# Kernel optimization log

Measured on AMD Instinct MI355X. Metric: run time of the kernel, lower is better.

Reference implementation:

```python
import jax, jax.numpy as jnp
import numpy as np

B, L = 64, 200
NQ = 1024          # n_question == output_dim
NPID = 4096
D = 256            # q_embed_dim
H = 512            # hidden_dim
Q = 1024           # output_dim
L2 = 1e-05


def setup_inputs() -> dict:
    key = jax.random.key(0)
    ks = jax.random.split(key, 20)
    q_data = jax.random.randint(ks[0], (B, L), 1, NQ + 1)          # question ids in [1, NQ]
    ans = jax.random.randint(ks[1], (B, L), 0, 2)
    qa_data = q_data + NQ * ans                                     # encoded (q, answer)
    pid_data = jax.random.randint(ks[2], (B, L), 0, NPID + 1)
    matrix = jax.random.uniform(ks[3], (Q, Q), jnp.float32) * 0.05  # p_c_relations
    u = jax.random.uniform(ks[4], (B, L))
    target = jnp.where(u < 0.1, -1.0, jnp.where(u < 0.55, 0.0, 1.0)).astype(jnp.float32)
    s = 0.05
    q_emb = jax.random.normal(ks[5], (NQ + 1, D), jnp.float32) * s
    qa_emb = jax.random.normal(ks[6], (2, D), jnp.float32) * s
    q_emb_diff = jax.random.normal(ks[7], (NQ + 1, D), jnp.float32) * s
    qa_emb_diff = jax.random.normal(ks[8], (2 * NQ + 1, D), jnp.float32) * s
    diff_parm = jax.random.normal(ks[9], (NPID + 1, 1), jnp.float32) * s
    gs = 1.0 / np.sqrt(H).astype(np.float32)
    w_ih = jax.random.uniform(ks[10], (3 * H, 2 * D), jnp.float32, -gs, gs)
    w_hh = jax.random.uniform(ks[11], (3 * H, H), jnp.float32, -gs, gs)
    b_ih = jax.random.uniform(ks[12], (3 * H,), jnp.float32, -gs, gs)
    b_hh = jax.random.uniform(ks[13], (3 * H,), jnp.float32, -gs, gs)
    fc_w = jax.random.normal(ks[14], (Q, H), jnp.float32) * 0.02
    fc_b = jnp.zeros((Q,), jnp.float32)
    return dict(q_data=q_data, qa_data=qa_data, pid_data=pid_data, matrix=matrix,
                target=target, q_emb=q_emb, qa_emb=qa_emb, q_emb_diff=q_emb_diff,
                qa_emb_diff=qa_emb_diff, diff_parm=diff_parm, w_ih=w_ih, w_hh=w_hh,
                b_ih=b_ih, b_hh=b_hh, fc_w=fc_w, fc_b=fc_b)


def _gru(x, w_ih, w_hh, b_ih, b_hh):
    # PyTorch GRU, single layer, batch_first. x: [B, L, In]
    xg = jnp.einsum('bli,gi->blg', x, w_ih) + b_ih          # [B, L, 3H]
    def step(h, xg_t):
        hg = h @ w_hh.T + b_hh
        xr, xz, xn = jnp.split(xg_t, 3, axis=-1)
        hr, hz, hn = jnp.split(hg, 3, axis=-1)
        r = jax.nn.sigmoid(xr + hr)
        z = jax.nn.sigmoid(xz + hz)
        n = jnp.tanh(xn + r * hn)
        h_new = (1.0 - z) * n + z * h
        return h_new, h_new
    h0 = jnp.zeros((x.shape[0], w_hh.shape[1]), x.dtype)
    _, hs = jax.lax.scan(step, h0, xg.transpose(1, 0, 2))
    return hs.transpose(1, 0, 2)                             # [B, L, H]


def reference(q_data, qa_data, pid_data, matrix, target, q_emb, qa_emb,
              q_emb_diff, qa_emb_diff, diff_parm, w_ih, w_hh, b_ih, b_hh,
              fc_w, fc_b):
    q_embed = q_emb[q_data]                                  # [B, L, D]
    qa = (qa_data - q_data) // NQ                            # answer in {0,1}
    qa_embed = qa_emb[qa] + q_embed
    pid_embed = diff_parm[pid_data]                          # [B, L, 1]
    q_embed2 = q_embed + pid_embed * q_emb_diff[q_data]
    qa_embed2 = qa_embed + pid_embed * qa_emb_diff[qa]
    c_reg = (pid_embed ** 2).sum() * L2

    x = jnp.concatenate([qa_embed2, q_embed2], axis=-1)      # [B, L, 2D]
    gru_out = _gru(x, w_ih, w_hh, b_ih, b_hh)
    gru_out = jnp.einsum('blh,qh->blq', gru_out, fc_w) + fc_b  # [B, L, Q]

    got = jnp.einsum('blq,kq->blk', gru_out, matrix)         # [B, L, Q]
    master = jnp.where(got >= 0.4, 1.0, got)                 # threshold-to-1 only
    # mastery of the question asked at step t: master[b, t, q-1]
    mvals = jnp.take_along_axis(master, (q_data - 1)[..., None], axis=2)[..., 0]  # [B, L]

    f32 = jnp.float32
    eq = (q_data[:, :, None] == q_data[:, None, :]).astype(f32)   # [B, t, k]
    t_idx = jnp.arange(L)
    tri_strict = (t_idx[:, None] > t_idx[None, :]).astype(f32)    # k < t
    tri_incl = (t_idx[:, None] >= t_idx[None, :]).astype(f32)     # k <= t
    mast = (mvals == 1.0).astype(f32)
    notm = (mvals == 0.0).astype(f32)
    qa1 = (qa == 1).astype(f32)
    qa0 = 1.0 - qa1
    base = eq * tri_strict                                        # [B, L, L]
    mc = jnp.einsum('btk,bk->bt', base, qa1 * mast)   # master_correct
    mi = jnp.einsum('btk,bk->bt', base, qa0 * mast)   # master_incorrect
    nmc = jnp.einsum('btk,bk->bt', base, qa0 * notm)  # no_master_correct
    aa = jnp.einsum('btk,tk->bt', eq, tri_incl)       # answered_all (>= 1)

    arB = jnp.arange(B)
    idx = q_data - 1

    def dina_step(carry, xs):
        guess, slip = carry                            # [B, Q] each
        i_t, m_t, qa_t, mc_t, mi_t, nmc_t, aa_t = xs   # [B] each
        g_upd = jnp.where(m_t == 1.0, mc_t / aa_t,
                          jnp.where(qa_t == 0, 1.0 - nmc_t / aa_t, nmc_t / aa_t))
        upd_slip = (m_t == 1.0) & (qa_t == 0)
        new_g = jnp.where(upd_slip, guess[arB, i_t], g_upd)
        new_s = jnp.where(upd_slip, mi_t / aa_t, slip[arB, i_t])
        guess = guess.at[arB, i_t].set(new_g)
        slip = slip.at[arB, i_t].set(new_s)
        p = (1.0 - new_s) * (m_t * new_g + (1.0 - new_s) * (1.0 - m_t))
        return (guess, slip), p

    init = (jnp.zeros((B, Q), f32), jnp.zeros((B, Q), f32))
    xs = (idx.T, mvals.T, qa.T, mc.T, mi.T, nmc.T, aa.T)
    _, ps = jax.lax.scan(dina_step, init, xs)          # [L, B]
    preds = ps.T.reshape(-1)                           # [B*L]

    labels = target.reshape(-1)
    mask = labels > -0.9
    preds_d = jax.lax.stop_gradient(preds)             # torch detaches via torch.tensor()
    mse_sum = (((preds_d - labels) ** 2) * mask.astype(f32)).sum()
    loss = mse_sum + c_reg
    return (loss, jax.nn.sigmoid(preds_d), mask.sum())
```

## Files before the change

kernel.cpp:

```cpp
#include <hip/hip_runtime.h>
#include <hip/hip_bf16.h>
#include <math.h>

#define BB 64
#define LL 200
#define NQ 1024
#define DD 256
#define HH 512
#define QQ 1024
#define G3 1536
#define BL 12800
#define GBLK 256

#define OFF_ACC   ((size_t)0)
#define OFF_CELLS ((size_t)16)
#define OFF_HA    ((size_t)1056)
#define OFF_AQ    (OFF_HA + 65536)
#define OFF_DQ    (OFF_AQ + 1574400)
#define OFF_BQA   (OFF_DQ + 1574400)
#define OFF_CQA   (OFF_BQA + 3072)
#define OFF_WSUM  (OFF_CQA + 3072)
#define OFF_FCWT  (OFF_WSUM + 393216)
#define OFF_M2    (OFF_FCWT + 524288)
#define OFF_MB    (OFF_M2 + 524288)
#define OFF_XG    (OFF_MB + 1024)
#define OFF_GRUT  (OFF_XG + 19660800)
#define OFF_QINT  (OFF_GRUT + 6553600)
#define OFF_QAINT (OFF_QINT + 12800)
#define OFF_PIDF  (OFF_QAINT + 12800)
#define OFF_MVAL  (OFF_PIDF + 12800)
#define OFF_MC    (OFF_MVAL + 12800)
#define OFF_MI    (OFF_MC + 12800)
#define OFF_NMC   (OFF_MI + 12800)
#define OFF_AA    (OFF_NMC + 12800)
#define OFF_PREDS (OFF_AA + 12800)

typedef float f32x4 __attribute__((ext_vector_type(4)));

__device__ __forceinline__ float wave_sum64(float v) {
    #pragma unroll
    for (int o = 32; o > 0; o >>= 1) v += __shfl_down(v, o, 64);
    return v;
}

__device__ __forceinline__ f32x4 llc_load4(const float* p) {
    f32x4 v;
    asm volatile("global_load_dwordx4 %0, %1, off sc0 sc1" : "=v"(v) : "v"(p));
    return v;
}
__device__ __forceinline__ void llc_wait2(f32x4& a, f32x4& b) {
    asm volatile("s_waitcnt vmcnt(0)" : "+v"(a), "+v"(b));
}
__device__ __forceinline__ void llc_store1(float* p, float v) {
    asm volatile("global_store_dword %0, %1, off sc0 sc1" :: "v"(p), "v"(v) : "memory");
}

__device__ __forceinline__ float quad_sum(float v) {
    float t1 = __int_as_float(__builtin_amdgcn_update_dpp(
        0, __float_as_int(v), 0xB1, 0xF, 0xF, true));
    v += t1;
    float t2 = __int_as_float(__builtin_amdgcn_update_dpp(
        0, __float_as_int(v), 0x4E, 0xF, 0xF, true));
    return v + t2;
}

__global__ __launch_bounds__(256) void prep_meta(
    const int* __restrict__ q_data, const int* __restrict__ qa_data,
    const int* __restrict__ pid_data, const float* __restrict__ diff_parm,
    int* __restrict__ qint, int* __restrict__ qaint, float* __restrict__ pidf,
    float* __restrict__ acc)
{
    int r = blockIdx.x * 256 + threadIdx.x;
    float pp = 0.f;
    if (r < BL) {
        int q = q_data[r];
        qint[r] = q;
        qaint[r] = (qa_data[r] - q) / NQ;
        float pid = diff_parm[pid_data[r]];
        pidf[r] = pid;
        pp = pid * pid;
    }
    pp = wave_sum64(pp);
    __shared__ float sm[4];
    int lane = threadIdx.x & 63, w = threadIdx.x >> 6;
    if (lane == 0) sm[w] = pp;
    __syncthreads();
    if (threadIdx.x == 0) atomicAdd(&acc[0], sm[0] + sm[1] + sm[2] + sm[3]);
}

__global__ __launch_bounds__(256) void wsum_kernel(const float* __restrict__ w_ih,
                                                   float* __restrict__ wsum)
{
    int g = blockIdx.x, d = threadIdx.x;
    wsum[(size_t)g * DD + d] = w_ih[(size_t)g * 2 * DD + d] + w_ih[(size_t)g * 2 * DD + DD + d];
}

__global__ __launch_bounds__(256) void gemm_nt_dual(
    const float* __restrict__ A0, const float* __restrict__ A1, int lda,
    const float* __restrict__ B0, const float* __restrict__ B1, int ldb0, int ldb1,
    float* __restrict__ C0, float* __restrict__ C1, int ldc,
    int M, int N, int K,
    const float* __restrict__ bias0, const float* __restrict__ bias1)
{
    const int z = blockIdx.z;
    const float* A = z ? A1 : A0;
    const float* B = z ? B1 : B0;
    float* C = z ? C1 : C0;
    const int ldb = z ? ldb1 : ldb0;
    const float* bias = z ? bias1 : bias0;

    __shared__ float As[16][129];
    __shared__ float Bs[16][65];
    const int bm = blockIdx.y * 128, bn = blockIdx.x * 64;
    const int tid = threadIdx.x;
    const int tx = tid & 15, ty = tid >> 4;
    const int mm = tid >> 4, kk = tid & 15;
    float acc[8][4] = {};
    float ar[8], br[4];
    #pragma unroll
    for (int i = 0; i < 8; ++i) {
        int m = bm + mm + 16 * i;
        ar[i] = (m < M) ? A[(size_t)m * lda + kk] : 0.f;
    }
    #pragma unroll
    for (int i = 0; i < 4; ++i) {
        int n = bn + mm + 16 * i;
        br[i] = (n < N) ? B[(size_t)n * ldb + kk] : 0.f;
    }
    for (int k0 = 0; k0 < K; k0 += 16) {
        #pragma unroll
        for (int i = 0; i < 8; ++i) As[kk][mm + 16 * i] = ar[i];
        #pragma unroll
        for (int i = 0; i < 4; ++i) Bs[kk][mm + 16 * i] = br[i];
        __syncthreads();
        int kn = k0 + 16;
        if (kn < K) {
            #pragma unroll
            for (int i = 0; i < 8; ++i) {
                int m = bm + mm + 16 * i;
                ar[i] = (m < M) ? A[(size_t)m * lda + kn + kk] : 0.f;
            }
            #pragma unroll
            for (int i = 0; i < 4; ++i) {
                int n = bn + mm + 16 * i;
                br[i] = (n < N) ? B[(size_t)n * ldb + kn + kk] : 0.f;
            }
        }
        #pragma unroll
        for (int kq = 0; kq < 16; ++kq) {
            float a[8], b[4];
            #pragma unroll
            for (int i = 0; i < 8; ++i) a[i] = As[kq][ty * 8 + i];
            #pragma unroll
            for (int j = 0; j < 4; ++j) b[j] = Bs[kq][tx * 4 + j];
            #pragma unroll
            for (int i = 0; i < 8; ++i)
                #pragma unroll
                for (int j = 0; j < 4; ++j) acc[i][j] += a[i] * b[j];
        }
        __syncthreads();
    }
    #pragma unroll
    for (int i = 0; i < 8; ++i) {
        int m = bm + ty * 8 + i;
        if (m >= M) continue;
        #pragma unroll
        for (int j = 0; j < 4; ++j) {
            int n = bn + tx * 4 + j;
            if (n >= N) continue;
            C[(size_t)m * ldc + n] = acc[i][j] + (bias ? bias[n] : 0.f);
        }
    }
}

__global__ __launch_bounds__(512) void m2mb_kernel(
    const float* __restrict__ matrix,
    const float* __restrict__ fc_w,
    const float* __restrict__ fc_b,
    float* __restrict__ M2,
    float* __restrict__ mb)
{
    __shared__ float As[16][65];
    __shared__ float Bs[16][65];
    const int tid = threadIdx.x;
    const int widx = blockIdx.x;
    if (widx >= 128) {
        const int wv2 = tid >> 6, lane2 = tid & 63;
        const int kb = (widx - 128) * 512 + wv2 * 64;
        for (int i = 0; i < 64; ++i) {
            const float* mrow = matrix + (size_t)(kb + i) * QQ;
            float sacc = 0.f;
            #pragma unroll
            for (int j = 0; j < 16; ++j)
                sacc += mrow[lane2 + 64 * j] * fc_b[lane2 + 64 * j];
            sacc = wave_sum64(sacc);
            if (lane2 == 0) mb[kb + i] = sacc;
        }
        return;
    }
    const int bm = (widx >> 3) * 64, bn = (widx & 7) * 64;
    const int mm = tid >> 4, kk = tid & 15;
    const int nn = tid & 31, k2 = tid >> 5;
    const int tx = tid & 15, ty = tid >> 4;
    float acc[2][4] = {};
    for (int k0 = 0; k0 < QQ; k0 += 16) {
        if (k0) __syncthreads();
        As[kk][mm]      = matrix[(size_t)(bm + mm) * QQ + k0 + kk];
        As[kk][mm + 32] = matrix[(size_t)(bm + mm + 32) * QQ + k0 + kk];
        Bs[k2][nn]      = fc_w[(size_t)(k0 + k2) * HH + bn + nn];
        Bs[k2][nn + 32] = fc_w[(size_t)(k0 + k2) * HH + bn + nn + 32];
        __syncthreads();
        #pragma unroll
        for (int kq = 0; kq < 16; ++kq) {
            float a0 = As[kq][ty * 2], a1 = As[kq][ty * 2 + 1];
            #pragma unroll
            for (int j = 0; j < 4; ++j) {
                float bv = Bs[kq][tx * 4 + j];
                acc[0][j] += a0 * bv;
                acc[1][j] += a1 * bv;
            }
        }
    }
    #pragma unroll
    for (int i = 0; i < 2; ++i)
        #pragma unroll
        for (int j = 0; j < 4; ++j)
            M2[(size_t)(bm + ty * 2 + i) * HH + bn + tx * 4 + j] = acc[i][j];
}

__global__ __launch_bounds__(512) void gru_persist(
    const float* __restrict__ Aq,
    const float* __restrict__ Dq,
    const float* __restrict__ Bqa,
    const float* __restrict__ Cqa,
    const int* __restrict__ qint,
    const int* __restrict__ qaint,
    const float* __restrict__ pidf,
    const float* __restrict__ w_hh,
    const float* __restrict__ b_hh,
    float* __restrict__ hA,
    float* __restrict__ gruT2,
    unsigned int* __restrict__ cells)
{
    __shared__ float hs[8][512];
    __shared__ float part[8][3][16][8];
    __shared__ float bqs[2][3][16];
    __shared__ float cqs[2][3][16];

    const int tid = threadIdx.x;
    const int bid = blockIdx.x;
    const int bg = bid >> 5;
    const int j0 = (bid & 31) * 16;
    const int wv = tid >> 6;
    const int lane = tid & 63;
    const int g = lane >> 2;
    const int s = lane & 3;

    if (tid < 96) {
        const int qa = tid / 48, rem = tid - qa * 48;
        const int gate = rem >> 4, u = rem & 15;
        bqs[qa][gate][u] = Bqa[(size_t)qa * G3 + gate * HH + j0 + u];
        cqs[qa][gate][u] = Cqa[(size_t)qa * G3 + gate * HH + j0 + u];
    }

    f32x4 ws4[3][4];
    #pragma unroll
    for (int gate = 0; gate < 3; ++gate)
        #pragma unroll
        for (int q = 0; q < 4; ++q)
            ws4[gate][q] = *(const f32x4*)&w_hh[
                (size_t)(gate * HH + j0 + g) * HH + wv * 64 + q * 16 + s * 4];

    const int eu = tid >> 3;
    const int eb = tid & 7;
    float bhr = 0.f, bhz = 0.f, bhn = 0.f;
    if (tid < 128) {
        bhr = b_hh[j0 + eu];
        bhz = b_hh[HH + j0 + eu];
        bhn = b_hh[2 * HH + j0 + eu];
    }

    const int b0 = lane >> 4;
    const int c0 = (lane & 15) * 4;

    __syncthreads();

    for (int t = 0; t < LL; ++t) {
        float xr = 0.f, xz = 0.f, xn = 0.f;
        if (tid < 128) {
            const int col = bg * 8 + eb;
            const int q = qint[col * LL + t];
            const int qa = qaint[col * LL + t];
            const float pid = pidf[col * LL + t];
            const float* aq = Aq + (size_t)q * G3 + j0 + eu;
            const float* dq = Dq + (size_t)q * G3 + j0 + eu;
            float ar_ = aq[0], az_ = aq[HH], an_ = aq[2 * HH];
            float dr_ = dq[0], dz_ = dq[HH], dn_ = dq[2 * HH];
            xr = ar_ + bqs[qa][0][eu] + pid * (cqs[qa][0][eu] + dr_);
            xz = az_ + bqs[qa][1][eu] + pid * (cqs[qa][1][eu] + dz_);
            xn = an_ + bqs[qa][2][eu] + pid * (cqs[qa][2][eu] + dn_);
        }
        if (t && tid < 64) {
            const unsigned want = (unsigned)t;
            for (;;) {
                unsigned v = want;
                if (lane < 32)
                    v = __hip_atomic_load(&cells[(bg * 32 + lane) * 4],
                                          __ATOMIC_RELAXED, __HIP_MEMORY_SCOPE_AGENT);
                if (__all((int)(v >= want))) break;
                __builtin_amdgcn_s_sleep(2);
            }
        }
        __syncthreads();

        {
            const float* hcur = hA + (size_t)(t & 1) * (HH * BB);
            const float* p0 = hcur + (size_t)(bg * 8 + b0) * HH + wv * 64 + c0;
            f32x4 va = llc_load4(p0);
            f32x4 vb = llc_load4(p0 + 4 * HH);
            llc_wait2(va, vb);
            *(f32x4*)&hs[wv][b0 * 64 + ((c0 + 8 * b0) & 63)] = va;
            *(f32x4*)&hs[wv][(b0 + 4) * 64 + ((c0 + 8 * b0 + 32) & 63)] = vb;
        }

        float acc[3][8];
        #pragma unroll
        for (int gate = 0; gate < 3; ++gate) {
            #pragma unroll
            for (int b = 0; b < 8; ++b) acc[gate][b] = 0.f;
        }
        #pragma unroll
        for (int q = 0; q < 4; ++q) {
            const int cb = q * 16 + s * 4;
            #pragma unroll
            for (int b = 0; b < 8; ++b) {
                f32x4 h4 = *(const f32x4*)&hs[wv][b * 64 + ((cb + 8 * b) & 63)];
                #pragma unroll
                for (int gate = 0; gate < 3; ++gate) {
                    acc[gate][b] += ws4[gate][q].x * h4.x + ws4[gate][q].y * h4.y
                                  + ws4[gate][q].z * h4.z + ws4[gate][q].w * h4.w;
                }
            }
        }

        #pragma unroll
        for (int gate = 0; gate < 3; ++gate)
            #pragma unroll
            for (int b = 0; b < 8; ++b)
                acc[gate][b] = quad_sum(acc[gate][b]);

        if (s < 3) {
            const int rot = (2 * ((g >> 2) + s)) & 7;
            #pragma unroll
            for (int hp = 0; hp < 4; ++hp) {
                const int b = hp * 2;
                float e0 = (s == 0) ? acc[0][b]     : (s == 1) ? acc[1][b]     : acc[2][b];
                float e1 = (s == 0) ? acc[0][b + 1] : (s == 1) ? acc[1][b + 1] : acc[2][b + 1];
                const int bp = (b + rot) & 7;
                *(float2*)&part[wv][s][g][bp] = make_float2(e0, e1);
            }
        }
        __syncthreads();

        if (tid < 128) {
            const int rb = eu >> 2;
            const int bp0 = (eb + 2 * (rb + 0)) & 7;
            const int bp1 = (eb + 2 * (rb + 1)) & 7;
            const int bp2 = (eb + 2 * (rb + 2)) & 7;
            float sg0 = 0.f, sg1 = 0.f, sg2 = 0.f;
            #pragma unroll
            for (int w = 0; w < 8; ++w) {
                sg0 += part[w][0][eu][bp0];
                sg1 += part[w][1][eu][bp1];
                sg2 += part[w][2][eu][bp2];
            }
            const int ku = j0 + eu;
            float hprev = hs[ku >> 6][eb * 64 + (((ku & 63) + 8 * eb) & 63)];
            float rg = 1.f / (1.f + expf(-(xr + sg0 + bhr)));
            float zg = 1.f / (1.f + expf(-(xz + sg1 + bhz)));
            float ng = tanhf(xn + rg * (sg2 + bhn));
            float hn = (1.f - zg) * ng + zg * hprev;
            llc_store1(hA + (size_t)((t + 1) & 1) * (HH * BB)
                          + (size_t)(bg * 8 + eb) * HH + ku, hn);
            gruT2[((size_t)t * BB + bg * 8 + eb) * HH + ku] = hn;
            asm volatile("s_waitcnt vmcnt(0)" ::: "memory");
        }
        __syncthreads();
        if (tid == 0 && t + 1 < LL)
            __hip_atomic_store(&cells[bid * 4], (unsigned)(t + 1),
                               __ATOMIC_RELAXED, __HIP_MEMORY_SCOPE_AGENT);
    }
}

__global__ __launch_bounds__(256) void mval_kernel(
    const float* __restrict__ gruT2,
    const float* __restrict__ M2,
    const float* __restrict__ mb,
    const int* __restrict__ qint,
    float* __restrict__ mval)
{
    int t = blockIdx.x;
    int wave = threadIdx.x >> 6, l = threadIdx.x & 63;
    for (int ii = 0; ii < 16; ++ii) {
        int b = wave * 16 + ii;
        int q = qint[b * LL + t] - 1;
        const float4* hp = (const float4*)(gruT2 + ((size_t)t * BB + b) * HH);
        const float4* mp = (const float4*)(M2 + (size_t)q * HH);
        float4 h0 = hp[l], m0 = mp[l];
        float4 h1 = hp[64 + l], m1 = mp[64 + l];
        float acc = h0.x * m0.x + h0.y * m0.y + h0.z * m0.z + h0.w * m0.w
                  + h1.x * m1.x + h1.y * m1.y + h1.z * m1.z + h1.w * m1.w;
        acc = wave_sum64(acc);
        if (l == 0) {
            float sv = acc + mb[q];
            mval[b * LL + t] = (sv >= 0.4f) ? 1.0f : sv;
        }
    }
}

__global__ __launch_bounds__(256) void stats_kernel(
    const int* __restrict__ qint, const int* __restrict__ qaint,
    const float* __restrict__ mval,
    float* __restrict__ mc, float* __restrict__ mi,
    float* __restrict__ nmc, float* __restrict__ aa)
{
    int b = blockIdx.x, tid = threadIdx.x;
    __shared__ int qs[LL];
    __shared__ int qas[LL];
    __shared__ float mv[LL];
    if (tid < LL) {
        qs[tid] = qint[b * LL + tid];
        qas[tid] = qaint[b * LL + tid];
        mv[tid] = mval[b * LL + tid];
    }
    __syncthreads();
    int t = tid;
    if (t < LL) {
        int qt = qs[t];
        float smc = 0.f, smi = 0.f, snmc = 0.f, saa = 0.f;
        for (int k = 0; k <= t; ++k) {
            if (qs[k] == qt) {
                saa += 1.f;
                if (k < t) {
                    float mk = (mv[k] == 1.f) ? 1.f : 0.f;
                    float nk = (mv[k] == 0.f) ? 1.f : 0.f;
                    float a1 = (qas[k] == 1) ? 1.f : 0.f;
                    smc += a1 * mk;
                    smi += (1.f - a1) * mk;
                    snmc += (1.f - a1) * nk;
                }
            }
        }
        mc[b * LL + t] = smc;
        mi[b * LL + t] = smi;
        nmc[b * LL + t] = snmc;
        aa[b * LL + t] = saa;
    }
}

__global__ __launch_bounds__(256) void dina_kernel(
    const int* __restrict__ qint, const int* __restrict__ qaint,
    const float* __restrict__ mval,
    const float* __restrict__ mc, const float* __restrict__ mi,
    const float* __restrict__ nmc, const float* __restrict__ aa,
    float* __restrict__ preds)
{
    int b = blockIdx.x, tid = threadIdx.x;
    __shared__ float guess[QQ], slip[QQ];
    __shared__ float s_m[LL], s_mc[LL], s_mi[LL], s_nmc[LL], s_aa[LL];
    __shared__ int s_i[LL], s_qa[LL];
    for (int i = tid; i < QQ; i += 256) { guess[i] = 0.f; slip[i] = 0.f; }
    if (tid < LL) {
        s_m[tid] = mval[b * LL + tid];
        s_mc[tid] = mc[b * LL + tid];
        s_mi[tid] = mi[b * LL + tid];
        s_nmc[tid] = nmc[b * LL + tid];
        s_aa[tid] = aa[b * LL + tid];
        s_i[tid] = qint[b * LL + tid] - 1;
        s_qa[tid] = qaint[b * LL + tid];
    }
    __syncthreads();
    if (tid == 0) {
        for (int t = 0; t < LL; ++t) {
            int i = s_i[t];
            float m = s_m[t];
            int qa = s_qa[t];
            float aat = s_aa[t];
            float g_upd = (m == 1.f) ? s_mc[t] / aat
                          : ((qa == 0) ? 1.f - s_nmc[t] / aat : s_nmc[t] / aat);
            bool us = (m == 1.f) && (qa == 0);
            float ng = us ? guess[i] : g_upd;
            float ns = us ? s_mi[t] / aat : slip[i];
            guess[i] = ng;
            slip[i] = ns;
            preds[b * LL + t] = (1.f - ns) * (m * ng + (1.f - ns) * (1.f - m));
        }
    }
}

__global__ __launch_bounds__(256) void loss_kernel(
    const float* __restrict__ preds, const float* __restrict__ target,
    float* __restrict__ out, float* __restrict__ acc)
{
    int r = blockIdx.x * 256 + threadIdx.x;
    float lm = 0.f, lc = 0.f;
    if (r < BL) {
        float p = preds[r], lab = target[r];
        float msk = (lab > -0.9f) ? 1.f : 0.f;
        float d = p - lab;
        lm = d * d * msk;
        lc = msk;
        out[1 + r] = 1.f / (1.f + expf(-p));
    }
    lm = wave_sum64(lm);
    lc = wave_sum64(lc);
    __shared__ float sm[4], sc[4];
    int lane = threadIdx.x & 63, w = threadIdx.x >> 6;
    if (lane == 0) { sm[w] = lm; sc[w] = lc; }
    __syncthreads();
    if (threadIdx.x == 0) {
        atomicAdd(&acc[1], sm[0] + sm[1] + sm[2] + sm[3]);
        atomicAdd(&acc[2], sc[0] + sc[1] + sc[2] + sc[3]);
    }
}

__global__ void final_kernel(const float* __restrict__ acc, float* __restrict__ out)
{
    out[0] = acc[1] + acc[0] * 1e-5f;
    out[1 + BL] = acc[2];
}

extern "C" void kernel_launch(void* const* d_in, const int* in_sizes, int n_in,
                              void* d_out, int out_size, void* d_ws, size_t ws_size,
                              hipStream_t stream) {
    const int* q_data = (const int*)d_in[0];
    const int* qa_data = (const int*)d_in[1];
    const int* pid_data = (const int*)d_in[2];
    const float* matrix = (const float*)d_in[3];
    const float* target = (const float*)d_in[4];
    const float* q_emb = (const float*)d_in[5];
    const float* qa_emb = (const float*)d_in[6];
    const float* q_emb_diff = (const float*)d_in[7];
    const float* qa_emb_diff = (const float*)d_in[8];
    const float* diff_parm = (const float*)d_in[9];
    const float* w_ih = (const float*)d_in[10];
    const float* w_hh = (const float*)d_in[11];
    const float* b_ih = (const float*)d_in[12];
    const float* b_hh = (const float*)d_in[13];
    const float* fc_w = (const float*)d_in[14];
    const float* fc_b = (const float*)d_in[15];
    float* out = (float*)d_out;
    float* W = (float*)d_ws;

    float* acc = W + OFF_ACC;
    unsigned int* cells = (unsigned int*)(W + OFF_CELLS);
    float* hA = W + OFF_HA;
    float* Aq = W + OFF_AQ;
    float* Dq = W + OFF_DQ;
    float* Bqa = W + OFF_BQA;
    float* Cqa = W + OFF_CQA;
    float* wsum = W + OFF_WSUM;
    float* M2 = W + OFF_M2;
    float* mb = W + OFF_MB;
    float* gruT2 = W + OFF_GRUT;
    int* qint = (int*)(W + OFF_QINT);
    int* qaint = (int*)(W + OFF_QAINT);
    float* pidf = W + OFF_PIDF;
    float* mval = W + OFF_MVAL;
    float* mc = W + OFF_MC;
    float* mi = W + OFF_MI;
    float* nmc = W + OFF_NMC;
    float* aa = W + OFF_AA;
    float* preds = W + OFF_PREDS;

    hipMemsetAsync(W, 0, (OFF_HA + 2 * HH * BB) * sizeof(float), stream);

    prep_meta<<<50, 256, 0, stream>>>(q_data, qa_data, pid_data, diff_parm,
                                      qint, qaint, pidf, acc);
    wsum_kernel<<<G3, 256, 0, stream>>>(w_ih, wsum);

    gemm_nt_dual<<<dim3(24, 1, 2), 256, 0, stream>>>(
        qa_emb, qa_emb_diff, DD, w_ih, w_ih, 2 * DD, 2 * DD,
        Bqa, Cqa, G3, 2, G3, DD, b_ih, nullptr);
    gemm_nt_dual<<<dim3(24, 9, 2), 256, 0, stream>>>(
        q_emb, q_emb_diff, DD, wsum, w_ih + DD, DD, 2 * DD,
        Aq, Dq, G3, NQ + 1, G3, DD, nullptr, nullptr);

    m2mb_kernel<<<130, 512, 0, stream>>>(matrix, fc_w, fc_b, M2, mb);

    gru_persist<<<GBLK, 512, 0, stream>>>(Aq, Dq, Bqa, Cqa, qint, qaint, pidf,
                                          w_hh, b_hh, hA, gruT2, cells);

    mval_kernel<<<LL, 256, 0, stream>>>(gruT2, M2, mb, qint, mval);
    stats_kernel<<<BB, 256, 0, stream>>>(qint, qaint, mval, mc, mi, nmc, aa);
    dina_kernel<<<BB, 256, 0, stream>>>(qint, qaint, mval, mc, mi, nmc, aa, preds);
    loss_kernel<<<50, 256, 0, stream>>>(preds, target, out, acc);
    final_kernel<<<1, 1, 0, stream>>>(acc, out);
}
```

Before: 1.151 ms.

## Fuse prep GEMMs, metadata and M2 into one launch; merge stats with DINA

Folds prep_meta, both embedding-projection GEMMs and the M2/mb product into a single prep_all kernel with block-index dispatch, so these independent pieces share one launch. The M2 GEMM is retiled for 256 threads with 4x4 outputs per thread. The GRU kernel now stages its per-step question, answer and pid indices in shared memory once instead of reading them from global memory every step. The stats and DINA kernels are merged, which removes one launch and the global round trip for mc/mi/nmc/aa. The cost is more shared memory per GRU block, which may lower occupancy.

```diff
diff --git a/kernel.cpp b/kernel.cpp
--- a/kernel.cpp
+++ b/kernel.cpp
@@ -64,30 +64,6 @@
     return v + t2;
 }
 
-__global__ __launch_bounds__(256) void prep_meta(
-    const int* __restrict__ q_data, const int* __restrict__ qa_data,
-    const int* __restrict__ pid_data, const float* __restrict__ diff_parm,
-    int* __restrict__ qint, int* __restrict__ qaint, float* __restrict__ pidf,
-    float* __restrict__ acc)
-{
-    int r = blockIdx.x * 256 + threadIdx.x;
-    float pp = 0.f;
-    if (r < BL) {
-        int q = q_data[r];
-        qint[r] = q;
-        qaint[r] = (qa_data[r] - q) / NQ;
-        float pid = diff_parm[pid_data[r]];
-        pidf[r] = pid;
-        pp = pid * pid;
-    }
-    pp = wave_sum64(pp);
-    __shared__ float sm[4];
-    int lane = threadIdx.x & 63, w = threadIdx.x >> 6;
-    if (lane == 0) sm[w] = pp;
-    __syncthreads();
-    if (threadIdx.x == 0) atomicAdd(&acc[0], sm[0] + sm[1] + sm[2] + sm[3]);
-}
-
 __global__ __launch_bounds__(256) void wsum_kernel(const float* __restrict__ w_ih,
                                                    float* __restrict__ wsum)
 {
@@ -95,24 +71,12 @@
     wsum[(size_t)g * DD + d] = w_ih[(size_t)g * 2 * DD + d] + w_ih[(size_t)g * 2 * DD + DD + d];
 }
 
-__global__ __launch_bounds__(256) void gemm_nt_dual(
-    const float* __restrict__ A0, const float* __restrict__ A1, int lda,
-    const float* __restrict__ B0, const float* __restrict__ B1, int ldb0, int ldb1,
-    float* __restrict__ C0, float* __restrict__ C1, int ldc,
-    int M, int N, int K,
-    const float* __restrict__ bias0, const float* __restrict__ bias1)
-{
-    const int z = blockIdx.z;
-    const float* A = z ? A1 : A0;
-    const float* B = z ? B1 : B0;
-    float* C = z ? C1 : C0;
-    const int ldb = z ? ldb1 : ldb0;
-    const float* bias = z ? bias1 : bias0;
-
-    __shared__ float As[16][129];
-    __shared__ float Bs[16][65];
-    const int bm = blockIdx.y * 128, bn = blockIdx.x * 64;
-    const int tid = threadIdx.x;
+__device__ __forceinline__ void gemm_nt_body(
+    const float* __restrict__ A, int lda, const float* __restrict__ B, int ldb,
+    float* __restrict__ C, int ldc, int M, int N, int K,
+    const float* __restrict__ bias, int bm, int bn, int tid,
+    float (*As)[129], float (*Bs)[65])
+{
     const int tx = tid & 15, ty = tid >> 4;
     const int mm = tid >> 4, kk = tid & 15;
     float acc[8][4] = {};
@@ -173,20 +137,85 @@
     }
 }
 
-__global__ __launch_bounds__(512) void m2mb_kernel(
-    const float* __restrict__ matrix,
-    const float* __restrict__ fc_w,
-    const float* __restrict__ fc_b,
-    float* __restrict__ M2,
-    float* __restrict__ mb)
-{
-    __shared__ float As[16][65];
+__global__ __launch_bounds__(256) void prep_all(
+    const float* __restrict__ q_emb, const float* __restrict__ q_emb_diff,
+    const float* __restrict__ qa_emb, const float* __restrict__ qa_emb_diff,
+    const float* __restrict__ wsum, const float* __restrict__ w_ih,
+    const float* __restrict__ b_ih,
+    float* __restrict__ Aq, float* __restrict__ Dq,
+    float* __restrict__ Bqa, float* __restrict__ Cqa,
+    const float* __restrict__ matrix, const float* __restrict__ fc_w,
+    const float* __restrict__ fc_b, float* __restrict__ M2, float* __restrict__ mb,
+    const int* __restrict__ q_data, const int* __restrict__ qa_data,
+    const int* __restrict__ pid_data, const float* __restrict__ diff_parm,
+    int* __restrict__ qint, int* __restrict__ qaint, float* __restrict__ pidf,
+    float* __restrict__ acc_g)
+{
+    __shared__ float As[16][129];
     __shared__ float Bs[16][65];
+    __shared__ float sm[4];
     const int tid = threadIdx.x;
     const int widx = blockIdx.x;
-    if (widx >= 128) {
+
+    if (widx < 432) {
+        const int z = widx >= 216;
+        const int w2 = z ? widx - 216 : widx;
+        const int bm = (w2 / 24) * 128, bn = (w2 % 24) * 64;
+        gemm_nt_body(z ? q_emb_diff : q_emb, DD,
+                     z ? (w_ih + DD) : wsum, z ? 2 * DD : DD,
+                     z ? Dq : Aq, G3, NQ + 1, G3, DD,
+                     nullptr, bm, bn, tid, As, Bs);
+        return;
+    }
+    if (widx < 480) {
+        const int w2 = widx - 432;
+        const int z = w2 >= 24;
+        const int bn = (z ? w2 - 24 : w2) * 64;
+        gemm_nt_body(z ? qa_emb_diff : qa_emb, DD,
+                     w_ih, 2 * DD,
+                     z ? Cqa : Bqa, G3, 2, G3, DD,
+                     z ? nullptr : b_ih, 0, bn, tid, As, Bs);
+        return;
+    }
+    if (widx < 608) {
+        const int w2 = widx - 480;
+        const int bm = (w2 >> 3) * 64, bn = (w2 & 7) * 64;
+        const int kk = tid & 15, mm = tid >> 4;
+        const int nb = tid & 63, kb2 = tid >> 6;
+        const int tx = tid & 15, ty = tid >> 4;
+        float acc[4][4] = {};
+        for (int k0 = 0; k0 < QQ; k0 += 16) {
+            if (k0) __syncthreads();
+            #pragma unroll
+            for (int i = 0; i < 4; ++i)
+                As[kk][mm + 16 * i] = matrix[(size_t)(bm + mm + 16 * i) * QQ + k0 + kk];
+            #pragma unroll
+            for (int i = 0; i < 4; ++i)
+                Bs[kb2 + 4 * i][nb] = fc_w[(size_t)(k0 + kb2 + 4 * i) * HH + bn + nb];
+            __syncthreads();
+            #pragma unroll
+            for (int kq = 0; kq < 16; ++kq) {
+                float a[4], b[4];
+                #pragma unroll
+                for (int i = 0; i < 4; ++i) a[i] = As[kq][ty * 4 + i];
+                #pragma unroll
+                for (int j = 0; j < 4; ++j) b[j] = Bs[kq][tx * 4 + j];
+                #pragma unroll
+                for (int i = 0; i < 4; ++i)
+                    #pragma unroll
+                    for (int j = 0; j < 4; ++j) acc[i][j] += a[i] * b[j];
+            }
+        }
+        #pragma unroll
+        for (int i = 0; i < 4; ++i)
+            #pragma unroll
+            for (int j = 0; j < 4; ++j)
+                M2[(size_t)(bm + ty * 4 + i) * HH + bn + tx * 4 + j] = acc[i][j];
+        return;
+    }
+    if (widx < 612) {
         const int wv2 = tid >> 6, lane2 = tid & 63;
-        const int kb = (widx - 128) * 512 + wv2 * 64;
+        const int kb = (widx - 608) * 256 + wv2 * 64;
         for (int i = 0; i < 64; ++i) {
             const float* mrow = matrix + (size_t)(kb + i) * QQ;
             float sacc = 0.f;
@@ -198,34 +227,23 @@
         }
         return;
     }
-    const int bm = (widx >> 3) * 64, bn = (widx & 7) * 64;
-    const int mm = tid >> 4, kk = tid & 15;
-    const int nn = tid & 31, k2 = tid >> 5;
-    const int tx = tid & 15, ty = tid >> 4;
-    float acc[2][4] = {};
-    for (int k0 = 0; k0 < QQ; k0 += 16) {
-        if (k0) __syncthreads();
-        As[kk][mm]      = matrix[(size_t)(bm + mm) * QQ + k0 + kk];
-        As[kk][mm + 32] = matrix[(size_t)(bm + mm + 32) * QQ + k0 + kk];
-        Bs[k2][nn]      = fc_w[(size_t)(k0 + k2) * HH + bn + nn];
-        Bs[k2][nn + 32] = fc_w[(size_t)(k0 + k2) * HH + bn + nn + 32];
+    {
+        int r = (widx - 612) * 256 + tid;
+        float pp = 0.f;
+        if (r < BL) {
+            int q = q_data[r];
+            qint[r] = q;
+            qaint[r] = (qa_data[r] - q) / NQ;
+            float pid = diff_parm[pid_data[r]];
+            pidf[r] = pid;
+            pp = pid * pid;
+        }
+        pp = wave_sum64(pp);
+        int lane = tid & 63, w = tid >> 6;
+        if (lane == 0) sm[w] = pp;
         __syncthreads();
-        #pragma unroll
-        for (int kq = 0; kq < 16; ++kq) {
-            float a0 = As[kq][ty * 2], a1 = As[kq][ty * 2 + 1];
-            #pragma unroll
-            for (int j = 0; j < 4; ++j) {
-                float bv = Bs[kq][tx * 4 + j];
-                acc[0][j] += a0 * bv;
-                acc[1][j] += a1 * bv;
-            }
-        }
-    }
-    #pragma unroll
-    for (int i = 0; i < 2; ++i)
-        #pragma unroll
-        for (int j = 0; j < 4; ++j)
-            M2[(size_t)(bm + ty * 2 + i) * HH + bn + tx * 4 + j] = acc[i][j];
+        if (tid == 0) atomicAdd(&acc_g[0], sm[0] + sm[1] + sm[2] + sm[3]);
+    }
 }
 
 __global__ __launch_bounds__(512) void gru_persist(
@@ -246,6 +264,9 @@
     __shared__ float part[8][3][16][8];
     __shared__ float bqs[2][3][16];
     __shared__ float cqs[2][3][16];
+    __shared__ int smq[8][200];
+    __shared__ int smqa[8][200];
+    __shared__ float smp[8][200];
 
     const int tid = threadIdx.x;
     const int bid = blockIdx.x;
@@ -262,6 +283,13 @@
         bqs[qa][gate][u] = Bqa[(size_t)qa * G3 + gate * HH + j0 + u];
         cqs[qa][gate][u] = Cqa[(size_t)qa * G3 + gate * HH + j0 + u];
     }
+    for (int i = tid; i < 8 * LL; i += 512) {
+        const int c = i / LL, tt = i - c * LL;
+        const int col = bg * 8 + c;
+        smq[c][tt] = qint[col * LL + tt];
+        smqa[c][tt] = qaint[col * LL + tt];
+        smp[c][tt] = pidf[col * LL + tt];
+    }
 
     f32x4 ws4[3][4];
     #pragma unroll
@@ -288,10 +316,9 @@
     for (int t = 0; t < LL; ++t) {
         float xr = 0.f, xz = 0.f, xn = 0.f;
         if (tid < 128) {
-            const int col = bg * 8 + eb;
-            const int q = qint[col * LL + t];
-            const int qa = qaint[col * LL + t];
-            const float pid = pidf[col * LL + t];
+            const int q = smq[eb][t];
+            const int qa = smqa[eb][t];
+            const float pid = smp[eb][t];
             const float* aq = Aq + (size_t)q * G3 + j0 + eu;
             const float* dq = Dq + (size_t)q * G3 + j0 + eu;
             float ar_ = aq[0], az_ = aq[HH], an_ = aq[2 * HH];
@@ -418,30 +445,29 @@
     }
 }
 
-__global__ __launch_bounds__(256) void stats_kernel(
+__global__ __launch_bounds__(256) void statsdina_kernel(
     const int* __restrict__ qint, const int* __restrict__ qaint,
-    const float* __restrict__ mval,
-    float* __restrict__ mc, float* __restrict__ mi,
-    float* __restrict__ nmc, float* __restrict__ aa)
+    const float* __restrict__ mval, float* __restrict__ preds)
 {
     int b = blockIdx.x, tid = threadIdx.x;
+    __shared__ float guess[QQ], slip[QQ];
     __shared__ int qs[LL];
     __shared__ int qas[LL];
-    __shared__ float mv[LL];
+    __shared__ float mv[LL], s_mc[LL], s_mi[LL], s_nmc[LL], s_aa[LL];
+    for (int i = tid; i < QQ; i += 256) { guess[i] = 0.f; slip[i] = 0.f; }
     if (tid < LL) {
         qs[tid] = qint[b * LL + tid];
         qas[tid] = qaint[b * LL + tid];
         mv[tid] = mval[b * LL + tid];
     }
     __syncthreads();
-    int t = tid;
-    if (t < LL) {
-        int qt = qs[t];
+    if (tid < LL) {
+        int qt = qs[tid];
         float smc = 0.f, smi = 0.f, snmc = 0.f, saa = 0.f;
-        for (int k = 0; k <= t; ++k) {
+        for (int k = 0; k <= tid; ++k) {
             if (qs[k] == qt) {
                 saa += 1.f;
-                if (k < t) {
+                if (k < tid) {
                     float mk = (mv[k] == 1.f) ? 1.f : 0.f;
                     float nk = (mv[k] == 0.f) ? 1.f : 0.f;
                     float a1 = (qas[k] == 1) ? 1.f : 0.f;
@@ -451,40 +477,17 @@
                 }
             }
         }
-        mc[b * LL + t] = smc;
-        mi[b * LL + t] = smi;
-        nmc[b * LL + t] = snmc;
-        aa[b * LL + t] = saa;
-    }
-}
-
-__global__ __launch_bounds__(256) void dina_kernel(
-    const int* __restrict__ qint, const int* __restrict__ qaint,
-    const float* __restrict__ mval,
-    const float* __restrict__ mc, const float* __restrict__ mi,
-    const float* __restrict__ nmc, const float* __restrict__ aa,
-    float* __restrict__ preds)
-{
-    int b = blockIdx.x, tid = threadIdx.x;
-    __shared__ float guess[QQ], slip[QQ];
-    __shared__ float s_m[LL], s_mc[LL], s_mi[LL], s_nmc[LL], s_aa[LL];
-    __shared__ int s_i[LL], s_qa[LL];
-    for (int i = tid; i < QQ; i += 256) { guess[i] = 0.f; slip[i] = 0.f; }
-    if (tid < LL) {
-        s_m[tid] = mval[b * LL + tid];
-        s_mc[tid] = mc[b * LL + tid];
-        s_mi[tid] = mi[b * LL + tid];
-        s_nmc[tid] = nmc[b * LL + tid];
-        s_aa[tid] = aa[b * LL + tid];
-        s_i[tid] = qint[b * LL + tid] - 1;
-        s_qa[tid] = qaint[b * LL + tid];
+        s_mc[tid] = smc;
+        s_mi[tid] = smi;
+        s_nmc[tid] = snmc;
+        s_aa[tid] = saa;
     }
     __syncthreads();
     if (tid == 0) {
         for (int t = 0; t < LL; ++t) {
-            int i = s_i[t];
-            float m = s_m[t];
-            int qa = s_qa[t];
+            int i = qs[t] - 1;
+            float m = mv[t];
+            int qa = qas[t];
             float aat = s_aa[t];
             float g_upd = (m == 1.f) ? s_mc[t] / aat
                           : ((qa == 0) ? 1.f - s_nmc[t] / aat : s_nmc[t] / aat);
@@ -567,33 +570,22 @@
     int* qaint = (int*)(W + OFF_QAINT);
     float* pidf = W + OFF_PIDF;
     float* mval = W + OFF_MVAL;
-    float* mc = W + OFF_MC;
-    float* mi = W + OFF_MI;
-    float* nmc = W + OFF_NMC;
-    float* aa = W + OFF_AA;
     float* preds = W + OFF_PREDS;
 
     hipMemsetAsync(W, 0, (OFF_HA + 2 * HH * BB) * sizeof(float), stream);
 
-    prep_meta<<<50, 256, 0, stream>>>(q_data, qa_data, pid_data, diff_parm,
-                                      qint, qaint, pidf, acc);
     wsum_kernel<<<G3, 256, 0, stream>>>(w_ih, wsum);
 
-    gemm_nt_dual<<<dim3(24, 1, 2), 256, 0, stream>>>(
-        qa_emb, qa_emb_diff, DD, w_ih, w_ih, 2 * DD, 2 * DD,
-        Bqa, Cqa, G3, 2, G3, DD, b_ih, nullptr);
-    gemm_nt_dual<<<dim3(24, 9, 2), 256, 0, stream>>>(
-        q_emb, q_emb_diff, DD, wsum, w_ih + DD, DD, 2 * DD,
-        Aq, Dq, G3, NQ + 1, G3, DD, nullptr, nullptr);
-
-    m2mb_kernel<<<130, 512, 0, stream>>>(matrix, fc_w, fc_b, M2, mb);
+    prep_all<<<662, 256, 0, stream>>>(
+        q_emb, q_emb_diff, qa_emb, qa_emb_diff, wsum, w_ih, b_ih,
+        Aq, Dq, Bqa, Cqa, matrix, fc_w, fc_b, M2, mb,
+        q_data, qa_data, pid_data, diff_parm, qint, qaint, pidf, acc);
 
     gru_persist<<<GBLK, 512, 0, stream>>>(Aq, Dq, Bqa, Cqa, qint, qaint, pidf,
                                           w_hh, b_hh, hA, gruT2, cells);
 
     mval_kernel<<<LL, 256, 0, stream>>>(gruT2, M2, mb, qint, mval);
-    stats_kernel<<<BB, 256, 0, stream>>>(qint, qaint, mval, mc, mi, nmc, aa);
-    dina_kernel<<<BB, 256, 0, stream>>>(qint, qaint, mval, mc, mi, nmc, aa, preds);
+    statsdina_kernel<<<BB, 256, 0, stream>>>(qint, qaint, mval, preds);
     loss_kernel<<<50, 256, 0, stream>>>(preds, target, out, acc);
     final_kernel<<<1, 1, 0, stream>>>(acc, out);
 }
```

New measurement: 1.075 ms. -6.6%, faster.
